# Kernel optimization log

Measured on AMD Instinct MI355X. Metric: run time of the kernel, lower is better.

Reference implementation:

```python
import jax, jax.numpy as jnp
import numpy as np

B, M, N, D, NOBJ, NV = 1024, 32, 64, 32, 20, 6890
K = M * N * 3  # 6144 offset dim


def setup_inputs() -> dict:
    key = jax.random.key(0)
    ks = jax.random.split(key, 7)
    return {
        "gamma": jax.random.normal(ks[0], (B, D), dtype=jnp.float32),
        "smpl_v": jax.random.normal(ks[1], (B, NV, 3), dtype=jnp.float32),
        "pca_components": jax.random.normal(ks[2], (NOBJ, D, K), dtype=jnp.float32) * 0.1,
        "pca_means": jax.random.normal(ks[3], (NOBJ, K), dtype=jnp.float32) * 0.1,
        "object_anchors": jax.random.normal(ks[4], (NOBJ, N, 3), dtype=jnp.float32),
        "object_labels": jax.random.randint(ks[5], (B,), 0, NOBJ, dtype=jnp.int64),
        "smpl_anchor_indices": jax.random.randint(ks[6], (M,), 0, NV, dtype=jnp.int64),
    }


def reference(gamma, smpl_v, pca_components, pca_means, object_anchors,
              object_labels, smpl_anchor_indices):
    b = gamma.shape[0]
    # --- decode: offsets = components^T @ gamma + mean (per-sample gather) ---
    comps = pca_components[object_labels]                      # [b, D, K]
    offsets = jnp.einsum('bdk,bd->bk', comps, gamma) + pca_means[object_labels]
    # --- decode_object_RT ---
    smpl_anchors = smpl_v[:, smpl_anchor_indices]              # [b, M, 3]
    oa = object_anchors[object_labels]                         # [b, N, 3]
    off = offsets.reshape(b, M, N, 3)
    P = (smpl_anchors[:, :, None, :] + off).reshape(b, M * N, 3)
    Q0 = jnp.broadcast_to(oa[:, None], (b, M, N, 3)).reshape(b, M * N, 3)
    center_Q = Q0.mean(axis=1, keepdims=True)                  # [b, 1, 3]
    Qc = Q0 - center_Q
    # 3x3 cross-covariance and Kabsch/Procrustes rotation
    H = jnp.einsum('bki,bkj->bij', P, Qc)                      # [b, 3, 3]
    u, s, vh = jnp.linalg.svd(H, full_matrices=False)
    det = jnp.linalg.det(jnp.einsum('bij,bjk->bik', u, vh))    # [b]
    d = jnp.concatenate([jnp.ones((b, 2), dtype=u.dtype), det[:, None]], axis=-1)
    R = jnp.einsum('bij,bj,bjk->bik', u, d, vh)                # [b, 3, 3]
    # translation: mean over points of P - R @ Q0
    T = (P - jnp.einsum('bij,bkj->bki', R, Q0)).mean(axis=1)   # [b, 3]
    return R.astype(gamma.dtype), T.astype(gamma.dtype)
```

## Files before the change

### kernel.cpp

```cpp
#include <hip/hip_runtime.h>
#include <math.h>

#define BB   1024
#define MM   32
#define NN   64
#define DD   32
#define NOBJ 20
#define NV   6890
#define KK   6144
#define JJ   192

__global__ void reduce_pca(const float* __restrict__ comps,
                           const float* __restrict__ means,
                           float* __restrict__ Cred,
                           float* __restrict__ Mred) {
    int t = blockIdx.x * blockDim.x + threadIdx.x;
    const int NC4 = NOBJ * DD * 48;
    if (t < NC4) {
        int jv = t % 48;
        int od = t / 48;
        const float4* p = reinterpret_cast<const float4*>(
            comps + (size_t)od * KK + jv * 4);
        float4 s = make_float4(0.f, 0.f, 0.f, 0.f);
#pragma unroll
        for (int m = 0; m < MM; ++m) {
            float4 v = p[m * 48];
            s.x += v.x; s.y += v.y; s.z += v.z; s.w += v.w;
        }
        reinterpret_cast<float4*>(Cred)[t] = s;
    } else {
        int t2 = t - NC4;
        if (t2 < NOBJ * 48) {
            int jv = t2 % 48;
            int o  = t2 / 48;
            const float4* p = reinterpret_cast<const float4*>(
                means + (size_t)o * KK + jv * 4);
            float4 s = make_float4(0.f, 0.f, 0.f, 0.f);
#pragma unroll
            for (int m = 0; m < MM; ++m) {
                float4 v = p[m * 48];
                s.x += v.x; s.y += v.y; s.z += v.z; s.w += v.w;
            }
            reinterpret_cast<float4*>(Mred)[t2] = s;
        }
    }
}

__global__ __launch_bounds__(192) void per_batch_H(
    const float* __restrict__ gamma,
    const float* __restrict__ smpl_v,
    const float* __restrict__ oanch,
    const int*   __restrict__ labels,
    const int*   __restrict__ sidx,
    const float* __restrict__ Cred,
    const float* __restrict__ Mred,
    float* __restrict__ Hc)
{
    const int b   = blockIdx.x;
    const int tid = threadIdx.x;

    __shared__ float s_gamma[DD];
    __shared__ float s_oa[JJ];
    __shared__ float s_off[JJ];
    __shared__ float s_sa[MM * 3];
    __shared__ float s_SA[3], s_c[3], s_sumoff[3];

    const int o = labels[b];

    if (tid < DD) s_gamma[tid] = gamma[b * DD + tid];
    if (tid < MM * 3) {
        int m = tid / 3, i = tid % 3;
        int v = sidx[m];
        s_sa[tid] = smpl_v[((size_t)b * NV + v) * 3 + i];
    }
    s_oa[tid] = oanch[o * JJ + tid];
    __syncthreads();

    {
        float acc = Mred[o * JJ + tid];
        const float* cp = Cred + (size_t)o * DD * JJ + tid;
#pragma unroll
        for (int d = 0; d < DD; ++d) acc += cp[d * JJ] * s_gamma[d];
        s_off[tid] = acc;
    }
    __syncthreads();

    if (tid < 3) {
        float sa = 0.f;
        for (int m = 0; m < MM; ++m) sa += s_sa[m * 3 + tid];
        s_SA[tid] = sa;
        float c = 0.f;
        for (int n = 0; n < NN; ++n) c += s_oa[n * 3 + tid];
        s_c[tid] = c * (1.0f / NN);
        float so = 0.f;
        for (int n = 0; n < NN; ++n) so += s_off[n * 3 + tid];
        s_sumoff[tid] = so;
    }
    __syncthreads();

    if (tid < 9) {
        int i = tid / 3, j = tid % 3;
        float cj = s_c[j];
        float h = 0.f;
        for (int n = 0; n < NN; ++n)
            h += s_off[n * 3 + i] * (s_oa[n * 3 + j] - cj);
        Hc[(size_t)b * 16 + tid] = h;
    }
    if (tid >= 9 && tid < 12) {
        Hc[(size_t)b * 16 + tid] = s_c[tid - 9];
    }
    if (tid >= 12 && tid < 15) {
        int i = tid - 12;
        Hc[(size_t)b * 16 + tid] =
            s_SA[i] * (1.0f / MM) + s_sumoff[i] * (1.0f / (MM * NN));
    }
}

__global__ __launch_bounds__(64) void solve(
    const float* __restrict__ Hc,
    float* __restrict__ out)
{
    const int b = blockIdx.x * 64 + threadIdx.x;
    const float* h = Hc + (size_t)b * 16;

    const float H00 = h[0], H01 = h[1], H02 = h[2];
    const float H10 = h[3], H11 = h[4], H12 = h[5];
    const float H20 = h[6], H21 = h[7], H22 = h[8];
    const float c0  = h[9], c1  = h[10], c2 = h[11];
    const float mP0 = h[12], mP1 = h[13], mP2 = h[14];

    float A[4][4], V[4][4];
    A[0][0] =  H00 + H11 + H22;
    A[1][1] =  H00 - H11 - H22;
    A[2][2] = -H00 + H11 - H22;
    A[3][3] = -H00 - H11 + H22;
    A[0][1] = A[1][0] = H21 - H12;
    A[0][2] = A[2][0] = H02 - H20;
    A[0][3] = A[3][0] = H10 - H01;
    A[1][2] = A[2][1] = H01 + H10;
    A[1][3] = A[3][1] = H02 + H20;
    A[2][3] = A[3][2] = H12 + H21;
#pragma unroll
    for (int r = 0; r < 4; ++r)
#pragma unroll
        for (int cc2 = 0; cc2 < 4; ++cc2) V[r][cc2] = (r == cc2) ? 1.f : 0.f;

    for (int sweep = 0; sweep < 8; ++sweep) {
#pragma unroll
        for (int p = 0; p < 3; ++p) {
#pragma unroll
            for (int q = p + 1; q < 4; ++q) {
                float apq  = A[p][q];
                float diff = A[q][q] - A[p][p];
                float sd   = (diff >= 0.f) ? 1.f : -1.f;
                float tt = 2.f * apq * sd /
                           (fabsf(diff) + sqrtf(diff * diff + 4.f * apq * apq)
                            + 1e-30f);
                float cc = 1.f / sqrtf(1.f + tt * tt);
                float ss = tt * cc;
#pragma unroll
                for (int k = 0; k < 4; ++k) {
                    float akp = A[k][p], akq = A[k][q];
                    A[k][p] = cc * akp - ss * akq;
                    A[k][q] = ss * akp + cc * akq;
                }
#pragma unroll
                for (int k = 0; k < 4; ++k) {
                    float apk = A[p][k], aqk = A[q][k];
                    A[p][k] = cc * apk - ss * aqk;
                    A[q][k] = ss * apk + cc * aqk;
                }
#pragma unroll
                for (int k = 0; k < 4; ++k) {
                    float vkp = V[k][p], vkq = V[k][q];
                    V[k][p] = cc * vkp - ss * vkq;
                    V[k][q] = ss * vkp + cc * vkq;
                }
            }
        }
    }

    float best = A[0][0];
    float w = V[0][0], x = V[1][0], y = V[2][0], z = V[3][0];
#pragma unroll
    for (int i = 1; i < 4; ++i) {
        bool gt = A[i][i] > best;
        best = gt ? A[i][i] : best;
        w = gt ? V[0][i] : w;
        x = gt ? V[1][i] : x;
        y = gt ? V[2][i] : y;
        z = gt ? V[3][i] : z;
    }
    float inv = 1.f / sqrtf(w * w + x * x + y * y + z * z);
    w *= inv; x *= inv; y *= inv; z *= inv;

    float R00 = w * w + x * x - y * y - z * z;
    float R01 = 2.f * (x * y - w * z);
    float R02 = 2.f * (x * z + w * y);
    float R10 = 2.f * (x * y + w * z);
    float R11 = w * w - x * x + y * y - z * z;
    float R12 = 2.f * (y * z - w * x);
    float R20 = 2.f * (x * z - w * y);
    float R21 = 2.f * (y * z + w * x);
    float R22 = w * w - x * x - y * y + z * z;

    float* Rout = out + (size_t)b * 9;
    Rout[0] = R00; Rout[1] = R01; Rout[2] = R02;
    Rout[3] = R10; Rout[4] = R11; Rout[5] = R12;
    Rout[6] = R20; Rout[7] = R21; Rout[8] = R22;

    float* Tout = out + (size_t)BB * 9 + (size_t)b * 3;
    Tout[0] = mP0 - (R00 * c0 + R01 * c1 + R02 * c2);
    Tout[1] = mP1 - (R10 * c0 + R11 * c1 + R12 * c2);
    Tout[2] = mP2 - (R20 * c0 + R21 * c1 + R22 * c2);
}

extern "C" void kernel_launch(void* const* d_in, const int* in_sizes, int n_in,
                              void* d_out, int out_size, void* d_ws, size_t ws_size,
                              hipStream_t stream) {
    const float* gamma  = (const float*)d_in[0];
    const float* smpl_v = (const float*)d_in[1];
    const float* comps  = (const float*)d_in[2];
    const float* means  = (const float*)d_in[3];
    const float* oanch  = (const float*)d_in[4];
    const int*   labels = (const int*)d_in[5];
    const int*   sidx   = (const int*)d_in[6];
    float* out = (float*)d_out;

    float* Cred = (float*)d_ws;
    float* Mred = Cred + NOBJ * DD * JJ;
    float* Hc   = Mred + NOBJ * JJ;

    const int total4 = NOBJ * DD * 48 + NOBJ * 48;
    reduce_pca<<<(total4 + 255) / 256, 256, 0, stream>>>(comps, means, Cred, Mred);
    per_batch_H<<<BB, JJ, 0, stream>>>(gamma, smpl_v, oanch, labels, sidx,
                                       Cred, Mred, Hc);
    solve<<<16, 64, 0, stream>>>(Hc, out);
}
```

Before: 147.5 us.

## Compute per-batch covariance with one wavefront and shuffle reductions

```diff
diff --git a/kernel.cpp b/kernel.cpp
--- a/kernel.cpp
+++ b/kernel.cpp
@@ -46,7 +46,7 @@
     }
 }
 
-__global__ __launch_bounds__(192) void per_batch_H(
+__global__ __launch_bounds__(64) void per_batch_H(
     const float* __restrict__ gamma,
     const float* __restrict__ smpl_v,
     const float* __restrict__ oanch,
@@ -56,63 +56,67 @@
     const float* __restrict__ Mred,
     float* __restrict__ Hc)
 {
-    const int b   = blockIdx.x;
-    const int tid = threadIdx.x;
-
-    __shared__ float s_gamma[DD];
+    const int b    = blockIdx.x;
+    const int lane = threadIdx.x;
+    const int o    = labels[b];
+
+    const int j0 = lane, j1 = lane + 64, j2 = lane + 128;
+
+    const float* Co = Cred + (size_t)o * DD * JJ;
+    const float* Mo = Mred + (size_t)o * JJ;
+    float off0 = Mo[j0], off1 = Mo[j1], off2 = Mo[j2];
+#pragma unroll
+    for (int d = 0; d < DD; ++d) {
+        float g = gamma[b * DD + d];
+        off0 += Co[d * JJ + j0] * g;
+        off1 += Co[d * JJ + j1] * g;
+        off2 += Co[d * JJ + j2] * g;
+    }
+
+    const float* Oo = oanch + (size_t)o * JJ;
+    float oa0 = Oo[j0], oa1 = Oo[j1], oa2 = Oo[j2];
+
+    float sax = 0.f, say = 0.f, saz = 0.f;
+    if (lane < MM) {
+        int v = sidx[lane];
+        const float* p = smpl_v + ((size_t)b * NV + v) * 3;
+        sax = p[0]; say = p[1]; saz = p[2];
+    }
+
+    __shared__ float s_off[JJ];
     __shared__ float s_oa[JJ];
-    __shared__ float s_off[JJ];
-    __shared__ float s_sa[MM * 3];
-    __shared__ float s_SA[3], s_c[3], s_sumoff[3];
-
-    const int o = labels[b];
-
-    if (tid < DD) s_gamma[tid] = gamma[b * DD + tid];
-    if (tid < MM * 3) {
-        int m = tid / 3, i = tid % 3;
-        int v = sidx[m];
-        s_sa[tid] = smpl_v[((size_t)b * NV + v) * 3 + i];
-    }
-    s_oa[tid] = oanch[o * JJ + tid];
+    s_off[j0] = off0; s_off[j1] = off1; s_off[j2] = off2;
+    s_oa[j0]  = oa0;  s_oa[j1]  = oa1;  s_oa[j2]  = oa2;
     __syncthreads();
 
-    {
-        float acc = Mred[o * JJ + tid];
-        const float* cp = Cred + (size_t)o * DD * JJ + tid;
-#pragma unroll
-        for (int d = 0; d < DD; ++d) acc += cp[d * JJ] * s_gamma[d];
-        s_off[tid] = acc;
-    }
-    __syncthreads();
-
-    if (tid < 3) {
-        float sa = 0.f;
-        for (int m = 0; m < MM; ++m) sa += s_sa[m * 3 + tid];
-        s_SA[tid] = sa;
-        float c = 0.f;
-        for (int n = 0; n < NN; ++n) c += s_oa[n * 3 + tid];
-        s_c[tid] = c * (1.0f / NN);
-        float so = 0.f;
-        for (int n = 0; n < NN; ++n) so += s_off[n * 3 + tid];
-        s_sumoff[tid] = so;
-    }
-    __syncthreads();
-
-    if (tid < 9) {
-        int i = tid / 3, j = tid % 3;
-        float cj = s_c[j];
-        float h = 0.f;
-        for (int n = 0; n < NN; ++n)
-            h += s_off[n * 3 + i] * (s_oa[n * 3 + j] - cj);
-        Hc[(size_t)b * 16 + tid] = h;
-    }
-    if (tid >= 9 && tid < 12) {
-        Hc[(size_t)b * 16 + tid] = s_c[tid - 9];
-    }
-    if (tid >= 12 && tid < 15) {
-        int i = tid - 12;
-        Hc[(size_t)b * 16 + tid] =
-            s_SA[i] * (1.0f / MM) + s_sumoff[i] * (1.0f / (MM * NN));
+    const int n = lane;
+    float p0 = s_off[n * 3 + 0], p1 = s_off[n * 3 + 1], p2 = s_off[n * 3 + 2];
+    float q0 = s_oa[n * 3 + 0],  q1 = s_oa[n * 3 + 1],  q2 = s_oa[n * 3 + 2];
+
+    float r0  = p0 * q0, r1  = p0 * q1, r2  = p0 * q2;
+    float r3  = p1 * q0, r4  = p1 * q1, r5  = p1 * q2;
+    float r6  = p2 * q0, r7  = p2 * q1, r8  = p2 * q2;
+
+#pragma unroll
+    for (int s = 1; s < 64; s <<= 1) {
+        r0 += __shfl_xor(r0, s); r1 += __shfl_xor(r1, s); r2 += __shfl_xor(r2, s);
+        r3 += __shfl_xor(r3, s); r4 += __shfl_xor(r4, s); r5 += __shfl_xor(r5, s);
+        r6 += __shfl_xor(r6, s); r7 += __shfl_xor(r7, s); r8 += __shfl_xor(r8, s);
+        p0 += __shfl_xor(p0, s); p1 += __shfl_xor(p1, s); p2 += __shfl_xor(p2, s);
+        q0 += __shfl_xor(q0, s); q1 += __shfl_xor(q1, s); q2 += __shfl_xor(q2, s);
+        sax += __shfl_xor(sax, s); say += __shfl_xor(say, s); saz += __shfl_xor(saz, s);
+    }
+    if (lane == 0) {
+        float c0 = q0 * (1.f / NN), c1 = q1 * (1.f / NN), c2 = q2 * (1.f / NN);
+        float* h = Hc + (size_t)b * 16;
+        h[0] = r0 - p0 * c0;  h[1] = r1 - p0 * c1;  h[2] = r2 - p0 * c2;
+        h[3] = r3 - p1 * c0;  h[4] = r4 - p1 * c1;  h[5] = r5 - p1 * c2;
+        h[6] = r6 - p2 * c0;  h[7] = r7 - p2 * c1;  h[8] = r8 - p2 * c2;
+        h[9]  = c0; h[10] = c1; h[11] = c2;
+        h[12] = sax * (1.f / MM) + p0 * (1.f / (MM * NN));
+        h[13] = say * (1.f / MM) + p1 * (1.f / (MM * NN));
+        h[14] = saz * (1.f / MM) + p2 * (1.f / (MM * NN));
+        h[15] = 0.f;
     }
 }
 
@@ -233,7 +237,7 @@
 
     const int total4 = NOBJ * DD * 48 + NOBJ * 48;
     reduce_pca<<<(total4 + 255) / 256, 256, 0, stream>>>(comps, means, Cred, Mred);
-    per_batch_H<<<BB, JJ, 0, stream>>>(gamma, smpl_v, oanch, labels, sidx,
+    per_batch_H<<<BB, 64, 0, stream>>>(gamma, smpl_v, oanch, labels, sidx,
                                        Cred, Mred, Hc);
     solve<<<16, 64, 0, stream>>>(Hc, out);
 }
```

Result: no change. 147.6 us (+0.1%).
